# Optimization experiments

Hardware: AMD Instinct MI355X
Metric: run time of the kernel (lower is better)

The kernel has to match this reference:

```python
import jax, jax.numpy as jnp
import numpy as np

B, S, D, H = 2, 2048, 1024, 16
HD = D // H
EPS = 1e-5


def setup_inputs() -> dict:
    key = jax.random.key(0)
    ks = jax.random.split(key, 8)
    std = 1.0 / np.sqrt(D)
    x = jax.random.normal(ks[0], (B, S, D), dtype=jnp.float32)
    # causal mask: True = attend (masked_fill where mask==0)
    attention_mask = jnp.tril(jnp.ones((S, S), dtype=bool))[None, None].repeat(B, axis=0)
    return {
        "x": x,
        "attention_mask": attention_mask,
        "ln_gamma": jnp.ones((D,), jnp.float32),
        "ln_beta": jnp.zeros((D,), jnp.float32),
        "w_qkv": jax.random.uniform(ks[1], (D, 3 * D), jnp.float32, -std, std),
        "b_qkv": jnp.zeros((3 * D,), jnp.float32),
        "w_gate": jax.random.uniform(ks[2], (D, D), jnp.float32, -std, std),
        "b_gate": jnp.zeros((D,), jnp.float32),
        "w_out": jax.random.uniform(ks[3], (D, D), jnp.float32, -std, std),
        "b_out": jnp.zeros((D,), jnp.float32),
        "rel_pos_bias": jnp.zeros((1, H, 1, 1), jnp.float32),
    }


def reference(x, attention_mask, ln_gamma, ln_beta, w_qkv, b_qkv,
              w_gate, b_gate, w_out, b_out, rel_pos_bias):
    # LayerNorm over model dim
    mu = jnp.mean(x, axis=-1, keepdims=True)
    var = jnp.mean(jnp.square(x - mu), axis=-1, keepdims=True)
    xn = (x - mu) * jax.lax.rsqrt(var + EPS) * ln_gamma + ln_beta

    qkv = xn @ w_qkv + b_qkv                      # [B,S,3D]
    qkv = qkv.reshape(B, S, 3, H, HD)
    q = qkv[:, :, 0].transpose(0, 2, 1, 3)        # [B,H,S,HD]
    k = qkv[:, :, 1].transpose(0, 2, 1, 3)
    v = qkv[:, :, 2].transpose(0, 2, 1, 3)

    u = jax.nn.silu(xn @ w_gate + b_gate)         # [B,S,D] SiLU gate

    scale = HD ** -0.5
    scores = jnp.einsum('bhqd,bhkd->bhqk', q * scale, k) + rel_pos_bias
    # masked_fill(mask==0, -inf) then sigmoid == zero out masked entries
    attn = jnp.where(attention_mask, jax.nn.sigmoid(scores), 0.0)
    ctx = jnp.einsum('bhqk,bhkd->bhqd', attn, v)  # [B,H,S,HD]
    ctx = ctx.transpose(0, 2, 1, 3).reshape(B, S, D)

    out = (ctx * u) @ w_out + b_out               # gated output proj
    return x + out                                # dropout=eval identity
```

## Files before the change

kernel.cpp:

```cpp
#include <hip/hip_runtime.h>
#include <hip/hip_bf16.h>
#include <cmath>

#define BB 2
#define SS 2048
#define DD 1024
#define HH 16
#define EPS 1e-5f
#define LOG2E 1.44269504088896f
#define QSCALE (0.125f * LOG2E)

typedef __attribute__((ext_vector_type(8))) short short8;
typedef __attribute__((ext_vector_type(4))) float f32x4;

__device__ inline unsigned short f2bf(float f) {
  union { float f; unsigned int u; } v; v.f = f;
  unsigned int u = v.u;
  unsigned int r = (u + 0x7FFFu + ((u >> 16) & 1u)) >> 16;
  return (unsigned short)r;
}
__device__ inline float bf2f(unsigned short h) {
  union { unsigned int u; float f; } v; v.u = ((unsigned int)h) << 16;
  return v.f;
}
__device__ inline unsigned short f2bf_fast(float f) {
  union { float f; unsigned int u; } v; v.f = f;
  return (unsigned short)((v.u + 0x8000u) >> 16);
}

__global__ __launch_bounds__(256) void ln_kernel(
    const float* __restrict__ x, const float* __restrict__ gamma,
    const float* __restrict__ beta, unsigned short* __restrict__ xn) {
  int row = blockIdx.x;
  int t = threadIdx.x;
  const float* xr = x + (size_t)row * DD;
  float4 v = *(const float4*)(xr + t * 4);
  float s = v.x + v.y + v.z + v.w;
  float sq = v.x * v.x + v.y * v.y + v.z * v.z + v.w * v.w;
  for (int off = 32; off > 0; off >>= 1) {
    s += __shfl_down(s, off, 64);
    sq += __shfl_down(sq, off, 64);
  }
  __shared__ float ls[4], lq[4];
  int wave = t >> 6, lane = t & 63;
  if (lane == 0) { ls[wave] = s; lq[wave] = sq; }
  __syncthreads();
  float tot = ls[0] + ls[1] + ls[2] + ls[3];
  float totq = lq[0] + lq[1] + lq[2] + lq[3];
  float mu = tot * (1.0f / DD);
  float var = totq * (1.0f / DD) - mu * mu;
  float rstd = rsqrtf(var + EPS);
  float4 g = *(const float4*)(gamma + t * 4);
  float4 bt = *(const float4*)(beta + t * 4);
  ushort4 o;
  o.x = f2bf((v.x - mu) * rstd * g.x + bt.x);
  o.y = f2bf((v.y - mu) * rstd * g.y + bt.y);
  o.z = f2bf((v.z - mu) * rstd * g.z + bt.z);
  o.w = f2bf((v.w - mu) * rstd * g.w + bt.w);
  *(ushort4*)(xn + (size_t)row * DD + t * 4) = o;
}

__global__ __launch_bounds__(256) void wtrans_all(
    const float* __restrict__ wq, const float* __restrict__ wg,
    const float* __restrict__ wo, unsigned short* __restrict__ wcatT,
    unsigned short* __restrict__ woutT) {
  __shared__ unsigned short tile[32][33];
  int bx = blockIdx.x;
  const float* W;
  unsigned short* Wt;
  int N, colbase;
  if (bx < 96)       { W = wq; Wt = wcatT; N = 3072; colbase = bx * 32; }
  else if (bx < 128) { W = wg; Wt = wcatT + (size_t)3072 * 1024; N = 1024; colbase = (bx - 96) * 32; }
  else               { W = wo; Wt = woutT; N = 1024; colbase = (bx - 128) * 32; }
  int by = blockIdx.y * 32;
  int tx = threadIdx.x & 31, ty = threadIdx.x >> 5;
#pragma unroll
  for (int i = 0; i < 32; i += 8)
    tile[ty + i][tx] = f2bf(W[(size_t)(by + ty + i) * N + colbase + tx]);
  __syncthreads();
#pragma unroll
  for (int i = 0; i < 32; i += 8)
    Wt[(size_t)(colbase + ty + i) * 1024 + by + tx] = tile[tx][ty + i];
}

__global__ __launch_bounds__(256) void gemm_qkvg(
    const unsigned short* __restrict__ A, const unsigned short* __restrict__ Bt,
    const float* __restrict__ bqkv, const float* __restrict__ bgate,
    unsigned short* __restrict__ qkb, unsigned short* __restrict__ vTb,
    unsigned short* __restrict__ ub) {
  __shared__ unsigned short SH[128 * 64];
  unsigned short* As = SH;
  unsigned short* Bs = SH + 128 * 32;
  const int K = 1024;
  int tid = threadIdx.x;
  int wave = tid >> 6, lane = tid & 63;
  int quad = lane >> 4, m16 = lane & 15;
  int wm = wave >> 1, wn = wave & 1;
  int m0 = blockIdx.y * 128, n0 = blockIdx.x * 128;

  int lrow = tid >> 2;
  int lcol = (tid & 3) * 8;
  const unsigned short* Ar0 = A + (size_t)(m0 + lrow) * K + lcol;
  const unsigned short* Ar1 = A + (size_t)(m0 + lrow + 64) * K + lcol;
  const unsigned short* Br0 = Bt + (size_t)(n0 + lrow) * K + lcol;
  const unsigned short* Br1 = Bt + (size_t)(n0 + lrow + 64) * K + lcol;

  f32x4 acc[4][4];
#pragma unroll
  for (int i = 0; i < 4; ++i)
#pragma unroll
    for (int j = 0; j < 4; ++j) acc[i][j] = (f32x4){0.f, 0.f, 0.f, 0.f};

  uint4 a0 = *(const uint4*)Ar0;
  uint4 a1 = *(const uint4*)Ar1;
  uint4 b0 = *(const uint4*)Br0;
  uint4 b1 = *(const uint4*)Br1;

  for (int k0 = 0; k0 < K; k0 += 32) {
    __syncthreads();
    *(uint4*)&As[lrow * 32 + lcol] = a0;
    *(uint4*)&As[(lrow + 64) * 32 + lcol] = a1;
    *(uint4*)&Bs[lrow * 32 + lcol] = b0;
    *(uint4*)&Bs[(lrow + 64) * 32 + lcol] = b1;
    __syncthreads();
    if (k0 + 32 < K) {
      a0 = *(const uint4*)(Ar0 + k0 + 32);
      a1 = *(const uint4*)(Ar1 + k0 + 32);
      b0 = *(const uint4*)(Br0 + k0 + 32);
      b1 = *(const uint4*)(Br1 + k0 + 32);
    }
    short8 af[4], bfr[4];
#pragma unroll
    for (int mi = 0; mi < 4; ++mi)
      af[mi] = *(const short8*)&As[(wm * 64 + mi * 16 + m16) * 32 + quad * 8];
#pragma unroll
    for (int ni = 0; ni < 4; ++ni)
      bfr[ni] = *(const short8*)&Bs[(wn * 64 + ni * 16 + m16) * 32 + quad * 8];
#pragma unroll
    for (int mi = 0; mi < 4; ++mi)
#pragma unroll
      for (int ni = 0; ni < 4; ++ni)
        acc[mi][ni] = __builtin_amdgcn_mfma_f32_16x16x32_bf16(
            af[mi], bfr[ni], acc[mi][ni], 0, 0, 0);
  }

  int sec = n0 >> 10;
  if (sec == 2) {
    int bat = m0 >> 11;
    int s_base = m0 & 2047;
    int dgbase = n0 - 2048;
#pragma unroll
    for (int p = 0; p < 2; ++p) {
      __syncthreads();
      if (wn == p) {
#pragma unroll
        for (int ni = 0; ni < 4; ++ni) {
          int dl = ni * 16 + m16;
          float bb = bqkv[2048 + dgbase + p * 64 + dl];
#pragma unroll
          for (int mi = 0; mi < 4; ++mi)
#pragma unroll
            for (int r = 0; r < 4; ++r) {
              int sl = wm * 64 + mi * 16 + quad * 4 + r;
              int sls = sl ^ ((dl & 7) << 4);
              SH[dl * 128 + sls] = f2bf(acc[mi][ni][r] + bb);
            }
        }
      }
      __syncthreads();
      int dl = tid >> 2;
      int dg = dgbase + p * 64 + dl;
      unsigned short* dst =
          vTb + ((size_t)(bat * 16 + (dg >> 6)) * 64 + (dg & 63)) * 2048 + s_base;
#pragma unroll
      for (int i = 0; i < 4; ++i) {
        int s0 = (tid & 3) * 8 + i * 32;
        int s0s = s0 ^ ((dl & 7) << 4);
        *(uint4*)(dst + s0) = *(const uint4*)&SH[dl * 128 + s0s];
      }
    }
  } else {
    int nwin = n0 + wn * 64;
    if (sec <= 1) {
      float qs = (sec == 0) ? QSCALE : 1.0f;
#pragma unroll
      for (int ni = 0; ni < 4; ++ni) {
        int col = nwin + ni * 16 + m16;
        float bb = bqkv[col];
#pragma unroll
        for (int mi = 0; mi < 4; ++mi)
#pragma unroll
          for (int r = 0; r < 4; ++r) {
            int row = m0 + wm * 64 + mi * 16 + quad * 4 + r;
            qkb[(size_t)row * 2048 + col] = f2bf((acc[mi][ni][r] + bb) * qs);
          }
      }
    } else {
#pragma unroll
      for (int ni = 0; ni < 4; ++ni) {
        int col = nwin + ni * 16 + m16;
        int g = col - 3072;
        float bb = bgate[g];
#pragma unroll
        for (int mi = 0; mi < 4; ++mi)
#pragma unroll
          for (int r = 0; r < 4; ++r) {
            int row = m0 + wm * 64 + mi * 16 + quad * 4 + r;
            float v = acc[mi][ni][r] + bb;
            v = v * __builtin_amdgcn_rcpf(1.0f + exp2f(-v * LOG2E));
            ub[(size_t)row * 1024 + g] = f2bf(v);
          }
      }
    }
  }
}

__global__ __launch_bounds__(256) void gemm_out(
    const unsigned short* __restrict__ A, const unsigned short* __restrict__ Bt,
    const float* __restrict__ bias, const float* __restrict__ resid,
    float* __restrict__ C) {
  __shared__ unsigned short As[128 * 32];
  __shared__ unsigned short Bs[128 * 32];
  const int K = 1024, N = 1024;
  int tid = threadIdx.x;
  int wave = tid >> 6, lane = tid & 63;
  int quad = lane >> 4, m16 = lane & 15;
  int wm = wave >> 1, wn = wave & 1;
  int m0 = blockIdx.y * 128, n0 = blockIdx.x * 128;
  int lrow = tid >> 2;
  int lcol = (tid & 3) * 8;
  const unsigned short* Ar0 = A + (size_t)(m0 + lrow) * K + lcol;
  const unsigned short* Ar1 = A + (size_t)(m0 + lrow + 64) * K + lcol;
  const unsigned short* Br0 = Bt + (size_t)(n0 + lrow) * K + lcol;
  const unsigned short* Br1 = Bt + (size_t)(n0 + lrow + 64) * K + lcol;

  f32x4 acc[4][4];
#pragma unroll
  for (int i = 0; i < 4; ++i)
#pragma unroll
    for (int j = 0; j < 4; ++j) acc[i][j] = (f32x4){0.f, 0.f, 0.f, 0.f};

  uint4 a0 = *(const uint4*)Ar0;
  uint4 a1 = *(const uint4*)Ar1;
  uint4 b0 = *(const uint4*)Br0;
  uint4 b1 = *(const uint4*)Br1;

  for (int k0 = 0; k0 < K; k0 += 32) {
    __syncthreads();
    *(uint4*)&As[lrow * 32 + lcol] = a0;
    *(uint4*)&As[(lrow + 64) * 32 + lcol] = a1;
    *(uint4*)&Bs[lrow * 32 + lcol] = b0;
    *(uint4*)&Bs[(lrow + 64) * 32 + lcol] = b1;
    __syncthreads();
    if (k0 + 32 < K) {
      a0 = *(const uint4*)(Ar0 + k0 + 32);
      a1 = *(const uint4*)(Ar1 + k0 + 32);
      b0 = *(const uint4*)(Br0 + k0 + 32);
      b1 = *(const uint4*)(Br1 + k0 + 32);
    }
    short8 af[4], bfr[4];
#pragma unroll
    for (int mi = 0; mi < 4; ++mi)
      af[mi] = *(const short8*)&As[(wm * 64 + mi * 16 + m16) * 32 + quad * 8];
#pragma unroll
    for (int ni = 0; ni < 4; ++ni)
      bfr[ni] = *(const short8*)&Bs[(wn * 64 + ni * 16 + m16) * 32 + quad * 8];
#pragma unroll
    for (int mi = 0; mi < 4; ++mi)
#pragma unroll
      for (int ni = 0; ni < 4; ++ni)
        acc[mi][ni] = __builtin_amdgcn_mfma_f32_16x16x32_bf16(
            af[mi], bfr[ni], acc[mi][ni], 0, 0, 0);
  }
#pragma unroll
  for (int ni = 0; ni < 4; ++ni) {
    int col = n0 + wn * 64 + ni * 16 + m16;
    float bb = bias[col];
#pragma unroll
    for (int mi = 0; mi < 4; ++mi)
#pragma unroll
      for (int r = 0; r < 4; ++r) {
        int row = m0 + wm * 64 + mi * 16 + quad * 4 + r;
        C[(size_t)row * N + col] =
            acc[mi][ni][r] + bb + resid[(size_t)row * N + col];
      }
  }
}

__global__ __launch_bounds__(256) void attn_mfma(
    const unsigned short* __restrict__ qk, const unsigned short* __restrict__ vT,
    const unsigned short* __restrict__ u, const float* __restrict__ rpb,
    unsigned short* __restrict__ prod) {
  __shared__ unsigned short Qs[128 * 72];
  __shared__ unsigned short Ks[64 * 72];
  __shared__ unsigned short Vs[64 * 72];
  __shared__ unsigned short Ps[64 * 72];

  int qtA = blockIdx.x;
  int qtB = 31 - qtA;
  int q0A = qtA * 64, q0B = qtB * 64;
  int bh = blockIdx.y;
  int b = bh >> 4, h = bh & 15;
  int t = threadIdx.x;
  int wave = t >> 6, lane = t & 63;
  int quad = lane >> 4, m16 = lane & 15;

  const unsigned short* qbase = qk + (size_t)(b * SS) * 2048 + h * 64;
  const unsigned short* kbase = qbase + 1024;
  const unsigned short* vbase = vT + (size_t)bh * 64 * 2048;

  int row = t >> 3, blk8 = (t & 7) * 8;

  {
    const unsigned short* sA = qbase + (size_t)(q0A + row) * 2048 + blk8;
    const unsigned short* sB = qbase + (size_t)(q0B + row) * 2048 + blk8;
    *(uint4*)&Qs[row * 72 + blk8] = *(const uint4*)sA;
    *(uint4*)&Qs[(row + 32) * 72 + blk8] = *(const uint4*)(sA + (size_t)32 * 2048);
    *(uint4*)&Qs[(row + 64) * 72 + blk8] = *(const uint4*)sB;
    *(uint4*)&Qs[(row + 96) * 72 + blk8] = *(const uint4*)(sB + (size_t)32 * 2048);
  }

  f32x4 zero4 = {0.f, 0.f, 0.f, 0.f};
  f32x4 caccA[4], caccB[4];
#pragma unroll
  for (int nb = 0; nb < 4; ++nb) { caccA[nb] = zero4; caccB[nb] = zero4; }

  float hb2 = rpb[h] * LOG2E;
  int ktmax = qtB;
  int psw = quad << 3;
  int psr = ((m16 >> 2) & 3) << 3;

  for (int kt = 0; kt <= ktmax; ++kt) {
    int k0 = kt * 64;
    const unsigned short* kp = kbase + (size_t)(k0 + row) * 2048 + blk8;
    const unsigned short* vp = vbase + (size_t)row * 2048 + k0 + blk8;
    uint4 kv0 = *(const uint4*)kp;
    uint4 kv1 = *(const uint4*)(kp + (size_t)32 * 2048);
    uint4 vv0 = *(const uint4*)vp;
    uint4 vv1 = *(const uint4*)(vp + (size_t)32 * 2048);
    __syncthreads();
    *(uint4*)&Ks[row * 72 + blk8] = kv0;
    *(uint4*)&Ks[(row + 32) * 72 + blk8] = kv1;
    *(uint4*)&Vs[row * 72 + blk8] = vv0;
    *(uint4*)&Vs[(row + 32) * 72 + blk8] = vv1;
    __syncthreads();

    short8 kf[2][4], vf[2][4];
#pragma unroll
    for (int s = 0; s < 2; ++s)
#pragma unroll
      for (int nb = 0; nb < 4; ++nb) {
        kf[s][nb] = *(const short8*)&Ks[(nb * 16 + m16) * 72 + s * 32 + quad * 8];
        vf[s][nb] = *(const short8*)&Vs[(nb * 16 + m16) * 72 + s * 32 + quad * 8];
      }

#pragma unroll
    for (int tile = 0; tile < 2; ++tile) {
      if (tile == 1 && kt > qtA) break;
      int qlds = (tile == 0) ? (64 + wave * 16) : (wave * 16);
      int q0 = (tile == 0) ? q0B : q0A;
      bool diag = (tile == 0) ? (kt == qtB) : (kt == qtA);
      f32x4* cacc = (tile == 0) ? caccB : caccA;

      f32x4 sacc[4];
#pragma unroll
      for (int nb = 0; nb < 4; ++nb) sacc[nb] = zero4;
#pragma unroll
      for (int s = 0; s < 2; ++s) {
        short8 a = *(const short8*)&Qs[(qlds + m16) * 72 + s * 32 + quad * 8];
#pragma unroll
        for (int nb = 0; nb < 4; ++nb)
          sacc[nb] = __builtin_amdgcn_mfma_f32_16x16x32_bf16(a, kf[s][nb], sacc[nb], 0, 0, 0);
      }
#pragma unroll
      for (int nb = 0; nb < 4; ++nb) {
#pragma unroll
        for (int r = 0; r < 4; ++r) {
          float y = sacc[nb][r] + hb2;
          float p = __builtin_amdgcn_rcpf(1.0f + exp2f(-y));
          if (diag) {
            int key = k0 + nb * 16 + m16;
            int q = q0 + wave * 16 + quad * 4 + r;
            if (key > q) p = 0.f;
          }
          int colS = (nb * 16 + m16) ^ psw;
          Ps[(wave * 16 + quad * 4 + r) * 72 + colS] = f2bf_fast(p);
        }
      }
#pragma unroll
      for (int s = 0; s < 2; ++s) {
        int pcol = (s * 32 + quad * 8) ^ psr;
        short8 a = *(const short8*)&Ps[(wave * 16 + m16) * 72 + pcol];
#pragma unroll
        for (int nb = 0; nb < 4; ++nb)
          cacc[nb] = __builtin_amdgcn_mfma_f32_16x16x32_bf16(a, vf[s][nb], cacc[nb], 0, 0, 0);
      }
    }
  }

  const unsigned short* ub_ = u + (size_t)(b * SS) * 1024 + h * 64;
  unsigned short* pb_ = prod + (size_t)(b * SS) * 1024 + h * 64;
#pragma unroll
  for (int nb = 0; nb < 4; ++nb) {
    int d = nb * 16 + m16;
#pragma unroll
    for (int r = 0; r < 4; ++r) {
      int qA = q0A + wave * 16 + quad * 4 + r;
      int qB = q0B + wave * 16 + quad * 4 + r;
      pb_[(size_t)qA * 1024 + d] = f2bf(caccA[nb][r] * bf2f(ub_[(size_t)qA * 1024 + d]));
      pb_[(size_t)qB * 1024 + d] = f2bf(caccB[nb][r] * bf2f(ub_[(size_t)qB * 1024 + d]));
    }
  }
}

extern "C" void kernel_launch(void* const* d_in, const int* in_sizes, int n_in,
                              void* d_out, int out_size, void* d_ws, size_t ws_size,
                              hipStream_t stream) {
  const float* x      = (const float*)d_in[0];
  const float* gamma  = (const float*)d_in[2];
  const float* beta   = (const float*)d_in[3];
  const float* w_qkv  = (const float*)d_in[4];
  const float* b_qkv  = (const float*)d_in[5];
  const float* w_gate = (const float*)d_in[6];
  const float* b_gate = (const float*)d_in[7];
  const float* w_out  = (const float*)d_in[8];
  const float* b_out  = (const float*)d_in[9];
  const float* rpb    = (const float*)d_in[10];
  float* out = (float*)d_out;

  unsigned short* xnb   = (unsigned short*)d_ws;
  unsigned short* qkb   = xnb + 4194304;
  unsigned short* vTb   = qkb + 8388608;
  unsigned short* ub    = vTb + 4194304;
  unsigned short* prodb = ub + 4194304;
  unsigned short* wcatT = prodb + 4194304;
  unsigned short* woutT = wcatT + 4194304;

  ln_kernel<<<BB * SS, 256, 0, stream>>>(x, gamma, beta, xnb);
  wtrans_all<<<dim3(160, 32), 256, 0, stream>>>(w_qkv, w_gate, w_out, wcatT, woutT);
  gemm_qkvg<<<dim3(4096 / 128, 4096 / 128), 256, 0, stream>>>(
      xnb, wcatT, b_qkv, b_gate, qkb, vTb, ub);
  attn_mfma<<<dim3(16, BB * HH), 256, 0, stream>>>(qkb, vTb, ub, rpb, prodb);
  gemm_out<<<dim3(1024 / 128, 4096 / 128), 256, 0, stream>>>(
      prodb, woutT, b_out, x, out);
}
```

Baseline: 251.1 us.

## Prefetch next K/V tile into registers, keep Q in registers, read K/V fragments per-use

The attention kernel now issues the next K/V tile's global loads into registers right after the current tile is stored to LDS, so the loads overlap with the current tile's MFMA work. Q fragments are loaded straight from global memory into registers, which removes the Q shared-memory buffer. K/V fragments are read from LDS at each use instead of being cached for the whole tile, and the bias add is folded into a precomputed exp2 constant. Together these cut LDS footprint and register pressure and hide global latency, at the cost of repeated LDS reads when both query tiles are processed.

```diff
diff --git a/kernel.cpp b/kernel.cpp
--- a/kernel.cpp
+++ b/kernel.cpp
@@ -291,7 +291,6 @@
     const unsigned short* __restrict__ qk, const unsigned short* __restrict__ vT,
     const unsigned short* __restrict__ u, const float* __restrict__ rpb,
     unsigned short* __restrict__ prod) {
-  __shared__ unsigned short Qs[128 * 72];
   __shared__ unsigned short Ks[64 * 72];
   __shared__ unsigned short Vs[64 * 72];
   __shared__ unsigned short Ps[64 * 72];
@@ -311,13 +310,11 @@
 
   int row = t >> 3, blk8 = (t & 7) * 8;
 
-  {
-    const unsigned short* sA = qbase + (size_t)(q0A + row) * 2048 + blk8;
-    const unsigned short* sB = qbase + (size_t)(q0B + row) * 2048 + blk8;
-    *(uint4*)&Qs[row * 72 + blk8] = *(const uint4*)sA;
-    *(uint4*)&Qs[(row + 32) * 72 + blk8] = *(const uint4*)(sA + (size_t)32 * 2048);
-    *(uint4*)&Qs[(row + 64) * 72 + blk8] = *(const uint4*)sB;
-    *(uint4*)&Qs[(row + 96) * 72 + blk8] = *(const uint4*)(sB + (size_t)32 * 2048);
+  short8 qfA[2], qfB[2];
+#pragma unroll
+  for (int s = 0; s < 2; ++s) {
+    qfA[s] = *(const short8*)(qbase + (size_t)(q0A + wave * 16 + m16) * 2048 + s * 32 + quad * 8);
+    qfB[s] = *(const short8*)(qbase + (size_t)(q0B + wave * 16 + m16) * 2048 + s * 32 + quad * 8);
   }
 
   f32x4 zero4 = {0.f, 0.f, 0.f, 0.f};
@@ -326,38 +323,43 @@
   for (int nb = 0; nb < 4; ++nb) { caccA[nb] = zero4; caccB[nb] = zero4; }
 
   float hb2 = rpb[h] * LOG2E;
+  float cexp = exp2f(-hb2);
   int ktmax = qtB;
   int psw = quad << 3;
   int psr = ((m16 >> 2) & 3) << 3;
 
+  uint4 kv0, kv1, vv0, vv1;
+  {
+    const unsigned short* kp = kbase + (size_t)row * 2048 + blk8;
+    const unsigned short* vp = vbase + (size_t)row * 2048 + blk8;
+    kv0 = *(const uint4*)kp;
+    kv1 = *(const uint4*)(kp + (size_t)32 * 2048);
+    vv0 = *(const uint4*)vp;
+    vv1 = *(const uint4*)(vp + (size_t)32 * 2048);
+  }
+
   for (int kt = 0; kt <= ktmax; ++kt) {
     int k0 = kt * 64;
-    const unsigned short* kp = kbase + (size_t)(k0 + row) * 2048 + blk8;
-    const unsigned short* vp = vbase + (size_t)row * 2048 + k0 + blk8;
-    uint4 kv0 = *(const uint4*)kp;
-    uint4 kv1 = *(const uint4*)(kp + (size_t)32 * 2048);
-    uint4 vv0 = *(const uint4*)vp;
-    uint4 vv1 = *(const uint4*)(vp + (size_t)32 * 2048);
     __syncthreads();
     *(uint4*)&Ks[row * 72 + blk8] = kv0;
     *(uint4*)&Ks[(row + 32) * 72 + blk8] = kv1;
     *(uint4*)&Vs[row * 72 + blk8] = vv0;
     *(uint4*)&Vs[(row + 32) * 72 + blk8] = vv1;
     __syncthreads();
-
-    short8 kf[2][4], vf[2][4];
-#pragma unroll
-    for (int s = 0; s < 2; ++s)
-#pragma unroll
-      for (int nb = 0; nb < 4; ++nb) {
-        kf[s][nb] = *(const short8*)&Ks[(nb * 16 + m16) * 72 + s * 32 + quad * 8];
-        vf[s][nb] = *(const short8*)&Vs[(nb * 16 + m16) * 72 + s * 32 + quad * 8];
-      }
+    if (kt < ktmax) {
+      int k0n = k0 + 64;
+      const unsigned short* kp = kbase + (size_t)(k0n + row) * 2048 + blk8;
+      const unsigned short* vp = vbase + (size_t)row * 2048 + k0n + blk8;
+      kv0 = *(const uint4*)kp;
+      kv1 = *(const uint4*)(kp + (size_t)32 * 2048);
+      vv0 = *(const uint4*)vp;
+      vv1 = *(const uint4*)(vp + (size_t)32 * 2048);
+    }
 
 #pragma unroll
     for (int tile = 0; tile < 2; ++tile) {
       if (tile == 1 && kt > qtA) break;
-      int qlds = (tile == 0) ? (64 + wave * 16) : (wave * 16);
+      const short8* qf = (tile == 0) ? qfB : qfA;
       int q0 = (tile == 0) ? q0B : q0A;
       bool diag = (tile == 0) ? (kt == qtB) : (kt == qtA);
       f32x4* cacc = (tile == 0) ? caccB : caccA;
@@ -367,17 +369,18 @@
       for (int nb = 0; nb < 4; ++nb) sacc[nb] = zero4;
 #pragma unroll
       for (int s = 0; s < 2; ++s) {
-        short8 a = *(const short8*)&Qs[(qlds + m16) * 72 + s * 32 + quad * 8];
-#pragma unroll
-        for (int nb = 0; nb < 4; ++nb)
-          sacc[nb] = __builtin_amdgcn_mfma_f32_16x16x32_bf16(a, kf[s][nb], sacc[nb], 0, 0, 0);
+#pragma unroll
+        for (int nb = 0; nb < 4; ++nb) {
+          short8 bf = *(const short8*)&Ks[(nb * 16 + m16) * 72 + s * 32 + quad * 8];
+          sacc[nb] = __builtin_amdgcn_mfma_f32_16x16x32_bf16(qf[s], bf, sacc[nb], 0, 0, 0);
+        }
       }
 #pragma unroll
       for (int nb = 0; nb < 4; ++nb) {
 #pragma unroll
         for (int r = 0; r < 4; ++r) {
-          float y = sacc[nb][r] + hb2;
-          float p = __builtin_amdgcn_rcpf(1.0f + exp2f(-y));
+          float e = exp2f(-sacc[nb][r]);
+          float p = __builtin_amdgcn_rcpf(fmaf(cexp, e, 1.0f));
           if (diag) {
             int key = k0 + nb * 16 + m16;
             int q = q0 + wave * 16 + quad * 4 + r;
@@ -392,8 +395,10 @@
         int pcol = (s * 32 + quad * 8) ^ psr;
         short8 a = *(const short8*)&Ps[(wave * 16 + m16) * 72 + pcol];
 #pragma unroll
-        for (int nb = 0; nb < 4; ++nb)
-          cacc[nb] = __builtin_amdgcn_mfma_f32_16x16x32_bf16(a, vf[s][nb], cacc[nb], 0, 0, 0);
+        for (int nb = 0; nb < 4; ++nb) {
+          short8 bf = *(const short8*)&Vs[(nb * 16 + m16) * 72 + s * 32 + quad * 8];
+          cacc[nb] = __builtin_amdgcn_mfma_f32_16x16x32_bf16(a, bf, cacc[nb], 0, 0, 0);
+        }
       }
     }
   }
```

Result: faster. 245.1 us (-2.4%).
